# Performance work log

Hardware: AMD Instinct MI355X
Metric: run time of the kernel (lower is better)

Reference implementation:

```python
import jax, jax.numpy as jnp
import numpy as np

ROT = 8
EPS = 1e-5


def _rot_offsets(ks, r):
    # integer-rounded rotated kernel tap offsets, exactly as cal_rot_pad
    c = (ks - 1) / 2
    locx = np.array([[j - c for j in range(ks)] for _ in range(ks)])
    locy = np.array([[i - c for _ in range(ks)] for i in range(ks)])
    loc = np.concatenate((locx.reshape(-1, 1), locy.reshape(-1, 1)), axis=1)  # [ks*ks, (x,y)]
    offs = []
    for i in range(r):
        th = 2.0 * np.pi / r * i
        R = np.array([[np.cos(th), -np.sin(th)], [np.sin(th), np.cos(th)]])
        offs.append(np.around(loc @ R).astype(np.int64))
    m = int(max(int(o.max()) for o in offs))
    return offs, m


def _build_rot_kernel(w, offs, m, r, separate):
    # w: [oc_r, cin, ks, ks]. The torch per-angle pad+cat+1x1conv+crop equals a
    # zero-padded (2m+1)x(2m+1) conv whose kernel scatters w[o,row,col,cin] at
    # (m - y_rot, m - x_rot), accumulating rounding collisions. Non-separate
    # layers cyclically roll the r input-channel blocks by the rotation index.
    oc_r, cin, ks, _ = w.shape
    K = 2 * m + 1
    kers = []
    for i in range(r):
        if separate:
            wi = w
        else:
            wb = w.reshape(oc_r, r, cin // r, ks, ks)
            wi = jnp.roll(wb, i, axis=1).reshape(oc_r, cin, ks, ks)
        wflat = wi.reshape(oc_r, cin, ks * ks)  # row-major tap order matches offs
        l = offs[i]
        ker = jnp.zeros((oc_r, cin, K, K), w.dtype)
        ker = ker.at[:, :, m - l[:, 1], m - l[:, 0]].add(wflat)
        kers.append(ker)
    return jnp.concatenate(kers, axis=0)  # rotation-major out channels, like torch.cat


def _conv(x, w, pad):
    return jax.lax.conv_general_dilated(
        x, w, (1, 1), [(pad, pad), (pad, pad)],
        dimension_numbers=('NCHW', 'OIHW', 'NCHW'))


def _rot_bn(x, gamma, beta, r):
    # training-mode BN applied independently to each rotation chunk, shared params
    B, C, H, W = x.shape
    xs = x.reshape(B, r, C // r, H, W)
    mu = xs.mean(axis=(0, 3, 4), keepdims=True)
    var = xs.var(axis=(0, 3, 4), keepdims=True)
    xn = (xs - mu) * jax.lax.rsqrt(var + EPS)
    xn = xn * gamma[None, None, :, None, None] + beta[None, None, :, None, None]
    return xn.reshape(B, C, H, W)


def _bn(x, gamma, beta):
    mu = x.mean(axis=(0, 2, 3), keepdims=True)
    var = x.var(axis=(0, 2, 3), keepdims=True)
    return (x - mu) * jax.lax.rsqrt(var + EPS) * gamma[None, :, None, None] + beta[None, :, None, None]


def _max_pool(x, k, pad=0):
    return jax.lax.reduce_window(
        x, -jnp.inf, jax.lax.max, (1, 1, k, k), (1, 1, k, k),
        [(0, 0), (0, 0), (pad, pad), (pad, pad)])


def _nms(x, r):
    # note: view is [B, C/r, r, H, W] (rotation-minor), exactly as the torch code
    B, C, H, W = x.shape
    xs = x.reshape(B, C // r, r, H, W)
    y = jnp.max(xs, axis=2, keepdims=True)
    mask = (y != xs).astype(x.dtype)
    return jnp.mean(xs * mask)


def _forward(x, w1, g1, b1, w2, g2, b2, w3, g3, b3,
             w4, g4, b4, w5, g5, b5, w6, g6, b6, w7, b7):
    offs, m = _rot_offsets(3, ROT)  # m == 1 for 3x3
    out = _conv(x, _build_rot_kernel(w1, offs, m, ROT, True), m)
    out = jax.nn.relu(_rot_bn(out, g1, b1, ROT))
    out = _conv(out, _build_rot_kernel(w2, offs, m, ROT, False), m)
    out = jax.nn.relu(_rot_bn(out, g2, b2, ROT))
    out = _max_pool(out, 2)
    out = _conv(out, _build_rot_kernel(w3, offs, m, ROT, False), m)
    out = jax.nn.relu(_rot_bn(out, g3, b3, ROT))
    n = _nms(out, ROT)
    out = jax.nn.relu(_bn(_conv(out, w4, 1), g4, b4))
    out = _max_pool(out, 2)
    out = jax.nn.relu(_bn(_conv(out, w5, 1), g5, b5))
    out = jax.nn.relu(_bn(_conv(out, w6, 1), g6, b6))
    out = _max_pool(out, 2, pad=1)
    out = _conv(out, w7, 2) + b7[None, :, None, None]
    out = _max_pool(out, out.shape[2])  # global max pool
    return out.reshape(out.shape[0], -1), n


def setup_inputs():
    key = jax.random.key(0)
    ks = jax.random.split(key, 24)
    f = jnp.float32
    d = {}
    d['x'] = jax.random.normal(ks[0], (2048, 1, 28, 28), f)
    wshapes = {'w1': (2, 1, 3, 3), 'w2': (2, 16, 3, 3), 'w3': (4, 16, 3, 3),
               'w4': (32, 32, 3, 3), 'w5': (64, 32, 3, 3), 'w6': (64, 64, 3, 3),
               'w7': (10, 64, 4, 4)}
    i = 1
    for name, sh in wshapes.items():
        d[name] = jax.random.normal(ks[i], sh, f) * 0.05
        i += 1
    bnc = {'1': 2, '2': 2, '3': 4, '4': 32, '5': 64, '6': 64}
    for suf, c in bnc.items():
        d['g' + suf] = 1.0 + 0.1 * jax.random.normal(ks[i], (c,), f)
        d['b' + suf] = 0.1 * jax.random.normal(ks[i + 1], (c,), f)
        i += 2
    d['b7'] = 0.1 * jax.random.normal(ks[i], (10,), f)
    return d


def reference(x, w1, w2, w3, w4, w5, w6, w7, g1, b1, g2, b2, g3, b3,
              g4, b4, g5, b5, g6, b6, b7):
    return _forward(x, w1, g1, b1, w2, g2, b2, w3, g3, b3,
                    w4, g4, b4, w5, g5, b5, w6, g6, b6, w7, b7)
```

## Files before the change

kernel.cpp:

```cpp
#include <hip/hip_runtime.h>

static constexpr int NB = 2048;
static constexpr float SENT = -1e30f;

typedef __attribute__((ext_vector_type(8))) short bf16x8;
typedef __attribute__((ext_vector_type(8))) unsigned short u16x8;
typedef __attribute__((ext_vector_type(4))) float f32x4;

#define ST_ADDR(base, ch, kind, copy) ((base) + (((ch)*4 + (copy))*32 + (kind)*8))

static constexpr int DST[8][9] = {
  {8,7,6,5,4,3,2,1,0},
  {5,8,7,2,4,6,1,0,3},
  {2,5,8,1,4,7,0,3,6},
  {1,2,5,0,4,8,3,6,7},
  {0,1,2,3,4,5,6,7,8},
  {3,0,1,6,4,2,7,8,5},
  {6,3,0,7,4,1,8,5,2},
  {7,6,3,8,4,0,5,2,1},
};

__device__ __forceinline__ unsigned short f2bf(float f){
  unsigned int u = __float_as_uint(f);
  u += 0x7fffu + ((u>>16)&1u);
  return (unsigned short)(u>>16);
}

__device__ __forceinline__ float bf2f(unsigned short h){
  return __uint_as_float((unsigned int)h << 16);
}

__device__ __forceinline__ unsigned int cvtpk(float lo, float hi){
  unsigned int r;
  asm("v_cvt_pk_bf16_f32 %0, %1, %2" : "=v"(r) : "v"(lo), "v"(hi));
  return r;
}

__device__ __forceinline__ unsigned int bnpair(unsigned int w, float a0, float b0, float a1, float b1){
  float vlo = __uint_as_float(w << 16);
  float vhi = __uint_as_float(w & 0xFFFF0000u);
  float r0 = fmaxf(vlo*a0 + b0, 0.f);
  float r1 = fmaxf(vhi*a1 + b1, 0.f);
  return cvtpk(r0, r1);
}

__device__ __forceinline__ float st_read(const float* base, int ch, int kind){
  return base[((ch*4+0)*32 + kind*8)] + base[((ch*4+1)*32 + kind*8)]
       + base[((ch*4+2)*32 + kind*8)] + base[((ch*4+3)*32 + kind*8)];
}

__device__ __forceinline__ int border_cell(int t){
  if (t<16) return t;
  if (t<32) return 240 + (t-16);
  if (t<46) return (t-31)*16;
  return (t-45)*16 + 15;
}

__global__ __launch_bounds__(256) void k_pre(const float* __restrict__ x, const float* __restrict__ w1,
                                             const float* __restrict__ w2, const float* __restrict__ w3,
                                             const float* __restrict__ w4,
                                             const float* __restrict__ w5, const float* __restrict__ w6,
                                             const float* __restrict__ w7,
                                             unsigned short* __restrict__ B2,
                                             unsigned short* __restrict__ B3,
                                             unsigned short* __restrict__ wb4,
                                             unsigned short* __restrict__ wb5, unsigned short* __restrict__ wb6,
                                             unsigned short* __restrict__ Bl,
                                             float* __restrict__ st){
  int blk = blockIdx.x;
  if (blk < 283){
    int i = blk*256 + threadIdx.x;
    if (i < 18432){
      int tap = i/2048, rem = i%2048, oc = rem/32, ci = rem%32;
      wb5[i] = f2bf(w5[(oc*32+ci)*9 + tap]);
    } else if (i < 55296){
      int j = i - 18432;
      int tap = j/4096, rem = j%4096, oc = rem/64, ci = rem%64;
      wb6[j] = f2bf(w6[(oc*64+ci)*9 + tap]);
    } else if (i < 64512){
      int j = i - 55296;
      int tap = j/1024, rem = j%1024, oc = rem/32, ci = rem%32;
      wb4[j] = f2bf(w4[(oc*32+ci)*9 + tap]);
    } else if (i < 67072){
      int j = i - 64512;
      int c = j >> 9;
      int rem = j & 511;
      int o = rem >> 5, k = rem & 31;
      int tap = c*2 + (k>>4);
      int ci = k & 15;
      unsigned short v = 0;
      if (tap <= 8){
        int rot = o>>1, u = o&1;
        int bb = ci>>1, ui = ci&1;
        int wc = (((bb - rot) & 7)<<1) | ui;
        int kk = 0;
        #pragma unroll
        for (int q=0;q<9;q++) if (DST[rot][q]==tap) kk=q;
        v = f2bf(w2[(u*16+wc)*9 + kk]);
      }
      B2[j] = v;
    } else if (i < 72192){
      int j = i - 67072;
      int c = j >> 10;
      int rem = j & 1023;
      int o = rem >> 5, k = rem & 31;
      int tap = c*2 + (k>>4);
      int ci = k & 15;
      unsigned short v = 0;
      if (tap <= 8){
        int rot = o>>2, uh = (o>>1)&1, ul = o&1;
        int bb = ci>>1, ui = ci&1;
        int wc = (((bb - rot) & 7)<<1) | ui;
        int kk = 0;
        #pragma unroll
        for (int q=0;q<9;q++) if (DST[rot][q]==tap) kk=q;
        v = f2bf(w3[uh*288 + (ul*16+wc)*9 + kk]);
      }
      B3[j] = v;
    }
    return;
  }
  if (blk < 1307){
    int i = (blk-283)*256 + threadIdx.x;
    int n = i>>10, k = i&1023;
    int pos16 = k>>6, ci = k&63;
    int r = pos16>>2, c = pos16&3;
    unsigned short v = 0;
    if (n < 250){
      int pos = n/10, o = n - 10*(n/10);
      int py = pos/5, px = pos - 5*(pos/5);
      int ky = r - py + 2, kx = c - px + 2;
      if (ky>=0 && ky<4 && kx>=0 && kx<4) v = f2bf(w7[(o*64+ci)*16 + ky*4 + kx]);
    }
    Bl[i] = v;
    return;
  }
  __shared__ float red[4][32];
  float wa[18];
  #pragma unroll
  for (int i=0;i<18;i++) wa[i] = w1[i];
  float s[16], s2[16];
  #pragma unroll
  for (int o=0;o<16;o++){ s[o]=0.f; s2[o]=0.f; }
  for (int idx = (blk-1307)*256 + threadIdx.x; idx < NB*784; idx += 512*256){
    int b = idx/784, pix = idx-b*784;
    int py = pix/28, px = pix-py*28;
    const float* xb = x + (size_t)b*784;
    float tap[9];
    #pragma unroll
    for (int d=0; d<9; d++){
      int dy = d/3-1, dx = d%3-1;
      int yy = py+dy, xx = px+dx;
      tap[d] = (yy>=0 && yy<28 && xx>=0 && xx<28) ? xb[yy*28+xx] : 0.f;
    }
    #pragma unroll
    for (int rot=0; rot<8; rot++){
      #pragma unroll
      for (int u=0; u<2; u++){
        float y = 0.f;
        #pragma unroll
        for (int k=0; k<9; k++) y += wa[u*9+k]*tap[DST[rot][k]];
        int ci = rot*2+u;
        s[ci] += y; s2[ci] += y*y;
      }
    }
  }
  int wid = threadIdx.x>>6;
  #pragma unroll
  for (int o=0;o<16;o++){
    float a = s[o], b2 = s2[o];
    #pragma unroll
    for (int off=32; off; off>>=1){ a += __shfl_down(a,off); b2 += __shfl_down(b2,off); }
    if ((threadIdx.x&63)==0){ red[wid][o] = a; red[wid][16+o] = b2; }
  }
  __syncthreads();
  if (threadIdx.x < 32){
    float v = red[0][threadIdx.x]+red[1][threadIdx.x]+red[2][threadIdx.x]+red[3][threadIdx.x];
    int ch = threadIdx.x & 15, kind = threadIdx.x >> 4;
    atomicAdd(ST_ADDR(st, ch, kind, blk & 3), v);
  }
}

template<int CI>
__global__ __launch_bounds__(64) void k_coef(const float* __restrict__ stin,
                                             const float* __restrict__ g, const float* __restrict__ be,
                                             float invN, int gmask,
                                             float* __restrict__ cf){
  int i = threadIdx.x;
  if (i < CI){
    float mu = st_read(stin, i, 0)*invN;
    float var = st_read(stin, i, 1)*invN - mu*mu;
    float a = g[i & gmask]*rsqrtf(var + 1e-5f);
    cf[i] = a; cf[CI + i] = be[i & gmask] - mu*a;
  }
}

__global__ __launch_bounds__(256, 2) void k_conv2m(const float* __restrict__ x,
                                                   const float* __restrict__ w1,
                                                   const unsigned short* __restrict__ B2,
                                                   const float* __restrict__ stin,
                                                   const float* __restrict__ g1, const float* __restrict__ b1,
                                                   unsigned short* __restrict__ p2b,
                                                   float* __restrict__ stout){
  __shared__ float smemf[8640];
  __shared__ float cab[32];
  __shared__ float red[4][32];
  unsigned short* Ls = (unsigned short*)smemf;
  float* xs = smemf + 7680;
  float* out2 = smemf;
  int t = threadIdx.x;
  int wid = t>>6, lane = t&63;
  int quad = lane>>4, m = lane&15;
  float wa[18];
  #pragma unroll
  for (int i=0;i<18;i++) wa[i] = w1[i];
  if (t < 16){
    const float invN = 1.f/1605632.f;
    float mu = st_read(stin, t, 0)*invN;
    float var = st_read(stin, t, 1)*invN - mu*mu;
    float a = g1[t&1]*rsqrtf(var + 1e-5f);
    cab[t] = a; cab[16+t] = b1[t&1] - mu*a;
  }
  int b = blockIdx.x;
  for (int i=t; i<960; i+=256){
    int r = i>>5, c = i&31;
    int iy = r-1, ix = c-1;
    xs[i] = (iy>=0 && iy<28 && ix>=0 && ix<28) ? x[(size_t)b*784 + iy*28 + ix] : 0.f;
  }
  for (int i=t; i<3840; i+=256) ((unsigned long long*)Ls)[i] = 0ULL;
  __syncthreads();
  for (int i=t; i<784; i+=256){
    int py = i/28, px = i - 28*(i/28);
    float tap[9];
    #pragma unroll
    for (int d=0; d<9; d++) tap[d] = xs[(py + d/3)*32 + px + d%3];
    float y[16];
    #pragma unroll
    for (int rot=0; rot<8; rot++){
      #pragma unroll
      for (int u=0; u<2; u++){
        float acc1 = 0.f;
        #pragma unroll
        for (int k=0; k<9; k++) acc1 += wa[u*9+k]*tap[DST[rot][k]];
        y[rot*2+u] = acc1;
      }
    }
    unsigned long long pk[4];
    #pragma unroll
    for (int q=0; q<4; q++){
      float4 A = *(const float4*)(cab + q*4);
      float4 Bv = *(const float4*)(cab + 16 + q*4);
      float r0 = fmaxf(y[q*4+0]*A.x + Bv.x, 0.f);
      float r1 = fmaxf(y[q*4+1]*A.y + Bv.y, 0.f);
      float r2 = fmaxf(y[q*4+2]*A.z + Bv.z, 0.f);
      float r3 = fmaxf(y[q*4+3]*A.w + Bv.w, 0.f);
      unsigned int lo = cvtpk(r0, r1);
      unsigned int hi = cvtpk(r2, r3);
      pk[q] = (unsigned long long)lo | ((unsigned long long)hi<<32);
    }
    int cell = (py+1)*32 + px + 1;
    unsigned long long* dstp = (unsigned long long*)(Ls + cell*16);
    dstp[0]=pk[0]; dstp[1]=pk[1]; dstp[2]=pk[2]; dstp[3]=pk[3];
  }
  __syncthreads();
  int jb[13];
  #pragma unroll
  for (int j=0;j<13;j++){
    int mt = wid + 4*j;
    int pos = (mt < 49) ? (mt*16 + m) : 0;
    int py = pos/28, px = pos - 28*py;
    jb[j] = (py*32 + px)*16 + (quad&1)*8;
  }
  f32x4 acc[13];
  #pragma unroll
  for (int j=0;j<13;j++) acc[j] = (f32x4){0.f,0.f,0.f,0.f};
  #pragma unroll
  for (int c=0;c<5;c++){
    const int tapA = 2*c, tapB = (2*c+1 < 9) ? 2*c+1 : 8;
    const int offA = ((tapA/3)*32 + tapA%3)*16;
    const int offB = ((tapB/3)*32 + tapB%3)*16;
    int sel = (quad < 2) ? offA : offB;
    bf16x8 Bf = *(const bf16x8*)(B2 + (c*16 + m)*32 + quad*8);
    #pragma unroll
    for (int j=0;j<13;j++){
      int mt = wid + 4*j;
      if (mt >= 49) continue;
      bf16x8 Af = *(const bf16x8*)(Ls + jb[j] + sel);
      acc[j] = __builtin_amdgcn_mfma_f32_16x16x32_bf16(Af, Bf, acc[j], 0, 0, 0);
    }
  }
  __syncthreads();
  float s = 0.f, sq = 0.f;
  #pragma unroll
  for (int j=0;j<13;j++){
    int mt = wid + 4*j;
    if (mt >= 49) continue;
    #pragma unroll
    for (int p=0;p<2;p++){
      int pos0 = mt*16 + quad*4 + p*2;
      float v0 = acc[j][2*p], v1 = acc[j][2*p+1];
      s += v0 + v1; sq += v0*v0 + v1*v1;
      float hm = fmaxf(v0, v1);
      int py = pos0/28, px2 = (pos0 - py*28)>>1;
      out2[(py*14+px2)*17 + m] = hm;
    }
  }
  s += __shfl_down(s,32);  s += __shfl_down(s,16);
  sq += __shfl_down(sq,32); sq += __shfl_down(sq,16);
  if (lane < 16){ red[wid][m] = s; red[wid][16+m] = sq; }
  __syncthreads();
  if (t < 32){
    float v = red[0][t]+red[1][t]+red[2][t]+red[3][t];
    int ch = t & 15, kind = t >> 4;
    atomicAdd(ST_ADDR(stout, ch, kind, b & 3), v);
  }
  unsigned short* pb = p2b + (size_t)b*4096;
  for (int i=t; i<3136; i+=256){
    int cell = i>>4, oc = i&15;
    int yo = cell/14, xo = cell - yo*14;
    float mx = fmaxf(out2[((2*yo)*14+xo)*17 + oc], out2[((2*yo+1)*14+xo)*17 + oc]);
    pb[((yo+1)*16 + xo + 1)*16 + oc] = f2bf(mx);
  }
  for (int i=t; i<960; i+=256){
    int bc = border_cell(i>>4), oc = i&15;
    pb[bc*16 + oc] = f2bf(SENT);
  }
}

__global__ __launch_bounds__(256, 2) void k_conv3w(const unsigned short* __restrict__ p2b,
                                                   const unsigned short* __restrict__ B3,
                                                   const float* __restrict__ stin,
                                                   const float* __restrict__ g2, const float* __restrict__ b2,
                                                   unsigned short* __restrict__ y3b,
                                                   float* __restrict__ stout){
  __shared__ unsigned short act[4][256*24];
  __shared__ float ca[16], cb[16];
  __shared__ float red[4][64];
  int t = threadIdx.x;
  int wid = t>>6, lane = t&63;
  int quad = lane>>4, m = lane&15;
  if (t < 16){
    const float invN = 1.f/1605632.f;
    float mu = st_read(stin, t, 0)*invN;
    float var = st_read(stin, t, 1)*invN - mu*mu;
    float a = g2[t&1]*rsqrtf(var + 1e-5f);
    ca[t] = a; cb[t] = b2[t&1] - mu*a;
  }
  __syncthreads();
  int b = blockIdx.x*4 + wid;
  unsigned short* A = act[wid];
  const unsigned short* sb = p2b + (size_t)b*4096;
  #pragma unroll
  for (int k=0;k<4;k++){
    int cell = lane + 64*k;
    uint4 U0 = *(const uint4*)(sb + cell*16);
    uint4 U1 = *(const uint4*)(sb + cell*16 + 8);
    unsigned int p0 = bnpair(U0.x, ca[0],cb[0], ca[1],cb[1]);
    unsigned int p1 = bnpair(U0.y, ca[2],cb[2], ca[3],cb[3]);
    unsigned int p2 = bnpair(U0.z, ca[4],cb[4], ca[5],cb[5]);
    unsigned int p3 = bnpair(U0.w, ca[6],cb[6], ca[7],cb[7]);
    unsigned int p4 = bnpair(U1.x, ca[8],cb[8], ca[9],cb[9]);
    unsigned int p5 = bnpair(U1.y, ca[10],cb[10], ca[11],cb[11]);
    unsigned int p6 = bnpair(U1.z, ca[12],cb[12], ca[13],cb[13]);
    unsigned int p7 = bnpair(U1.w, ca[14],cb[14], ca[15],cb[15]);
    unsigned long long* q = (unsigned long long*)(A + cell*24);
    q[0] = (unsigned long long)p0 | ((unsigned long long)p1<<32);
    q[1] = (unsigned long long)p2 | ((unsigned long long)p3<<32);
    q[2] = (unsigned long long)p4 | ((unsigned long long)p5<<32);
    q[3] = (unsigned long long)p6 | ((unsigned long long)p7<<32);
  }
  asm volatile("s_waitcnt lgkmcnt(0)" ::: "memory");
  __builtin_amdgcn_sched_barrier(0);
  int jpix[13];
  #pragma unroll
  for (int j=0;j<13;j++){
    int pos = j*16 + m;
    if (pos >= 196) pos = 0;
    int py = pos/14, px = pos - 14*(pos/14);
    jpix[j] = py*16 + px;
  }
  f32x4 acc[13][2];
  #pragma unroll
  for (int j=0;j<13;j++){ acc[j][0] = (f32x4){0,0,0,0}; acc[j][1] = (f32x4){0,0,0,0}; }
  int half = (quad&1)*8;
  #pragma unroll
  for (int c=0;c<5;c++){
    const int tapA = 2*c, tapB = (2*c+1 < 9) ? 2*c+1 : 8;
    const int offA = (tapA/3)*16 + tapA%3;
    const int offB = (tapB/3)*16 + tapB%3;
    int sel = (quad < 2) ? offA : offB;
    bf16x8 Bf0 = *(const bf16x8*)(B3 + (c*32 + m)*32 + quad*8);
    bf16x8 Bf1 = *(const bf16x8*)(B3 + (c*32 + 16 + m)*32 + quad*8);
    #pragma unroll
    for (int j=0;j<13;j++){
      bf16x8 Af = *(const bf16x8*)(A + (jpix[j] + sel)*24 + half);
      acc[j][0] = __builtin_amdgcn_mfma_f32_16x16x32_bf16(Af, Bf0, acc[j][0], 0, 0, 0);
      acc[j][1] = __builtin_amdgcn_mfma_f32_16x16x32_bf16(Af, Bf1, acc[j][1], 0, 0, 0);
    }
  }
  asm volatile("s_waitcnt lgkmcnt(0)" ::: "memory");
  __builtin_amdgcn_sched_barrier(0);
  unsigned short* yb = y3b + (size_t)b*8192;
  float s0=0.f, sq0=0.f, s1=0.f, sq1=0.f;
  #pragma unroll
  for (int j=0;j<13;j++){
    #pragma unroll
    for (int r=0;r<4;r++){
      int pos = j*16 + quad*4 + r;
      if (pos < 196){
        float v0 = acc[j][0][r], v1 = acc[j][1][r];
        int py2 = pos/14, px2 = pos - py2*14;
        int cell = (py2+1)*16 + px2 + 1;
        yb[cell*32 + m]      = f2bf(v0);
        yb[cell*32 + 16 + m] = f2bf(v1);
        s0 += v0; sq0 += v0*v0; s1 += v1; sq1 += v1*v1;
      }
    }
  }
  {
    unsigned short sh = f2bf(SENT);
    unsigned int SP = (unsigned int)sh | ((unsigned int)sh << 16);
    for (int i=lane; i<960; i+=64){
      int bc = border_cell(i>>4);
      int p = i & 15;
      *(unsigned int*)(yb + bc*32 + p*2) = SP;
    }
  }
  s0 += __shfl_down(s0,32); s0 += __shfl_down(s0,16);
  sq0 += __shfl_down(sq0,32); sq0 += __shfl_down(sq0,16);
  s1 += __shfl_down(s1,32); s1 += __shfl_down(s1,16);
  sq1 += __shfl_down(sq1,32); sq1 += __shfl_down(sq1,16);
  if (lane < 16){
    red[wid][m]      = s0;  red[wid][32+m]      = sq0;
    red[wid][16+m]   = s1;  red[wid][32+16+m]   = sq1;
  }
  __syncthreads();
  if (t < 64){
    float v = red[0][t]+red[1][t]+red[2][t]+red[3][t];
    int ch = t & 31, kind = t >> 5;
    atomicAdd(ST_ADDR(stout, ch, kind, blockIdx.x & 3), v);
  }
}

__global__ __launch_bounds__(256, 2) void k_conv4w(const unsigned short* __restrict__ y3b,
                                                   const unsigned short* __restrict__ wb4,
                                                   const float* __restrict__ stin,
                                                   const float* __restrict__ g3, const float* __restrict__ b3,
                                                   float* __restrict__ p4,
                                                   float* __restrict__ stout,
                                                   float* __restrict__ nmsa){
  __shared__ unsigned short act[4][8192];
  __shared__ float ca[32], cb[32];
  __shared__ float red[4][64];
  int t = threadIdx.x;
  int wid = t>>6, lane = t&63;
  int quad = lane>>4, m = lane&15;
  if (t < 32){
    const float invN = 1.f/401408.f;
    float mu = st_read(stin, t, 0)*invN;
    float var = st_read(stin, t, 1)*invN - mu*mu;
    float a = g3[t&3]*rsqrtf(var + 1e-5f);
    ca[t] = a; cb[t] = b3[t&3] - mu*a;
  }
  __syncthreads();
  int b = blockIdx.x*4 + wid;
  unsigned short* A = act[wid];
  const unsigned short* sb = y3b + (size_t)b*8192;
  #pragma unroll
  for (int k=0;k<4;k++){
    int cell = lane + 64*k;
    const uint4* src = (const uint4*)(sb + cell*32);
    int sw = cell & 3;
    unsigned short* dst = A + cell*32;
    #pragma unroll
    for (int c=0;c<4;c++){
      uint4 W = src[c];
      int c0 = c*8;
      unsigned int q0 = bnpair(W.x, ca[c0+0],cb[c0+0], ca[c0+1],cb[c0+1]);
      unsigned int q1 = bnpair(W.y, ca[c0+2],cb[c0+2], ca[c0+3],cb[c0+3]);
      unsigned int q2 = bnpair(W.z, ca[c0+4],cb[c0+4], ca[c0+5],cb[c0+5]);
      unsigned int q3 = bnpair(W.w, ca[c0+6],cb[c0+6], ca[c0+7],cb[c0+7]);
      unsigned long long* q = (unsigned long long*)(dst + ((c ^ sw)<<3));
      q[0] = (unsigned long long)q0 | ((unsigned long long)q1<<32);
      q[1] = (unsigned long long)q2 | ((unsigned long long)q3<<32);
    }
  }
  asm volatile("s_waitcnt lgkmcnt(0)" ::: "memory");
  __builtin_amdgcn_sched_barrier(0);
  float nloc = 0.f;
  for (int i=lane; i<784; i+=64){
    int hw = i>>2, c4 = i&3;
    int cell = (hw/14 + 1)*16 + hw%14 + 1;
    const unsigned int* g32 = (const unsigned int*)(A + cell*32 + ((c4 ^ (cell&3))<<3));
    unsigned int w0 = g32[0], w1 = g32[1], w2 = g32[2], w3 = g32[3];
    float v[8];
    v[0] = __uint_as_float(w0 << 16); v[1] = __uint_as_float(w0 & 0xFFFF0000u);
    v[2] = __uint_as_float(w1 << 16); v[3] = __uint_as_float(w1 & 0xFFFF0000u);
    v[4] = __uint_as_float(w2 << 16); v[5] = __uint_as_float(w2 & 0xFFFF0000u);
    v[6] = __uint_as_float(w3 << 16); v[7] = __uint_as_float(w3 & 0xFFFF0000u);
    float vmax = -1e30f;
    #pragma unroll
    for (int r=0;r<8;r++) vmax = fmaxf(vmax, v[r]);
    #pragma unroll
    for (int r=0;r<8;r++) nloc += (v[r] != vmax) ? v[r] : 0.f;
  }
  #pragma unroll
  for (int off=32; off; off>>=1) nloc += __shfl_down(nloc, off);
  if (lane == 0) atomicAdd(&nmsa[(b & 7)*32], nloc);
  int jc[13], jp[13];
  #pragma unroll
  for (int j=0;j<13;j++){
    int pos = j*16 + m;
    if (pos >= 196) pos = 0;
    int py = pos/14, px = pos - 14*(pos/14);
    jc[j] = py*16 + px;
    jp[j] = px;
  }
  f32x4 acc[13][2];
  #pragma unroll
  for (int j=0;j<13;j++){ acc[j][0] = (f32x4){0,0,0,0}; acc[j][1] = (f32x4){0,0,0,0}; }
  #pragma unroll
  for (int tap=0; tap<9; tap++){
    const int dy = tap/3, dx = tap - 3*(tap/3);
    bf16x8 Bf0 = *(const bf16x8*)(wb4 + (tap*32 + m)*32 + quad*8);
    bf16x8 Bf1 = *(const bf16x8*)(wb4 + (tap*32 + 16 + m)*32 + quad*8);
    #pragma unroll
    for (int j=0;j<13;j++){
      int ci = jc[j] + dy*16 + dx;
      int ph = quad ^ ((jp[j]+dx)&3);
      bf16x8 Af = *(const bf16x8*)(A + ci*32 + ph*8);
      acc[j][0] = __builtin_amdgcn_mfma_f32_16x16x32_bf16(Af, Bf0, acc[j][0], 0, 0, 0);
      acc[j][1] = __builtin_amdgcn_mfma_f32_16x16x32_bf16(Af, Bf1, acc[j][1], 0, 0, 0);
    }
  }
  asm volatile("s_waitcnt lgkmcnt(0)" ::: "memory");
  __builtin_amdgcn_sched_barrier(0);
  float* hp = (float*)A;
  float s0=0.f, sq0=0.f, s1=0.f, sq1=0.f;
  #pragma unroll
  for (int j=0;j<13;j++){
    #pragma unroll
    for (int p=0;p<2;p++){
      int pos0 = j*16 + quad*4 + 2*p;
      if (pos0 + 1 < 196){
        float a0 = acc[j][0][2*p], a1 = acc[j][0][2*p+1];
        float b0 = acc[j][1][2*p], b1 = acc[j][1][2*p+1];
        s0 += a0 + a1; sq0 += a0*a0 + a1*a1;
        s1 += b0 + b1; sq1 += b0*b0 + b1*b1;
        int py0 = pos0/14, pxh = (pos0 - py0*14)>>1;
        hp[(py0*7 + pxh)*33 + m]      = fmaxf(a0, a1);
        hp[(py0*7 + pxh)*33 + 16 + m] = fmaxf(b0, b1);
      }
    }
  }
  s0 += __shfl_down(s0,32); s0 += __shfl_down(s0,16);
  sq0 += __shfl_down(sq0,32); sq0 += __shfl_down(sq0,16);
  s1 += __shfl_down(s1,32); s1 += __shfl_down(s1,16);
  sq1 += __shfl_down(sq1,32); sq1 += __shfl_down(sq1,16);
  if (lane < 16){
    red[wid][m]      = s0;  red[wid][32+m]      = sq0;
    red[wid][16+m]   = s1;  red[wid][32+16+m]   = sq1;
  }
  asm volatile("s_waitcnt lgkmcnt(0)" ::: "memory");
  __builtin_amdgcn_sched_barrier(0);
  for (int i=lane; i<1568; i+=64){
    int cell = i>>5, oc = i&31;
    int yo = cell/7, xo = cell - yo*7;
    float mx = fmaxf(hp[((2*yo)*7 + xo)*33 + oc], hp[((2*yo+1)*7 + xo)*33 + oc]);
    p4[((size_t)b*49 + cell)*32 + oc] = mx;
  }
  __syncthreads();
  if (t < 64){
    float v = red[0][t]+red[1][t]+red[2][t]+red[3][t];
    int ch = t & 31, kind = t >> 5;
    atomicAdd(ST_ADDR(stout, ch, kind, blockIdx.x & 3), v);
  }
}

template<int CI>
__global__ __launch_bounds__(256, 2) void k_conv56m(const float* __restrict__ src,
                                                    const unsigned short* __restrict__ wb,
                                                    const float* __restrict__ stin,
                                                    const float* __restrict__ g, const float* __restrict__ be,
                                                    float invN,
                                                    float* __restrict__ dst,
                                                    float* __restrict__ stout){
  constexpr int CIP = CI + 8;
  constexpr int KC = CI/32;
  __shared__ unsigned short lin[4][81*CIP];
  __shared__ float red[4][256];
  __shared__ float ca[CI], cb[CI];
  int wid = threadIdx.x>>6, lane = threadIdx.x&63;
  int quad = lane>>4, m = lane&15;
  unsigned short* L = lin[wid];
  if (threadIdx.x < CI){
    int i = threadIdx.x;
    float mu = st_read(stin, i, 0)*invN;
    float var = st_read(stin, i, 1)*invN - mu*mu;
    float a = g[i]*rsqrtf(var + 1e-5f);
    ca[i] = a; cb[i] = be[i] - mu*a;
  }
  for (int i = lane; i < 81*CIP/4; i += 64) ((unsigned long long*)L)[i] = 0ULL;
  __syncthreads();
  int b = blockIdx.x*4 + wid;
  const float* sb = src + (size_t)b*49*CI;
  for (int i = lane; i < 49*CI/4; i += 64){
    int pos = i/(CI/4), cig = i - pos*(CI/4);
    float4 v = *(const float4*)(sb + pos*CI + cig*4);
    float r0 = fmaxf(v.x*ca[cig*4]  +cb[cig*4],   0.f);
    float r1 = fmaxf(v.y*ca[cig*4+1]+cb[cig*4+1], 0.f);
    float r2 = fmaxf(v.z*ca[cig*4+2]+cb[cig*4+2], 0.f);
    float r3 = fmaxf(v.w*ca[cig*4+3]+cb[cig*4+3], 0.f);
    int pos9 = (pos/7 + 1)*9 + pos%7 + 1;
    unsigned int lo = cvtpk(r0, r1);
    unsigned int hi = cvtpk(r2, r3);
    *(unsigned long long*)(L + pos9*CIP + cig*4) =
        (unsigned long long)lo | ((unsigned long long)hi<<32);
  }
  __syncthreads();
  int py[4], px[4];
  #pragma unroll
  for (int mt=0; mt<4; mt++){
    int pos = mt*16 + m;
    if (pos < 49){ py[mt] = pos/7; px[mt] = pos%7; }
    else { py[mt] = 0; px[mt] = 0; }
  }
  f32x4 acc[4][4];
  #pragma unroll
  for (int nt=0; nt<4; nt++)
    #pragma unroll
    for (int mt=0; mt<4; mt++) acc[nt][mt] = (f32x4){0.f,0.f,0.f,0.f};

  for (int tap=0; tap<9; tap++){
    int dy = tap/3, dx = tap - dy*3;
    int o9[4];
    #pragma unroll
    for (int mt=0; mt<4; mt++) o9[mt] = ((py[mt]+dy)*9 + px[mt]+dx)*CIP;
    #pragma unroll
    for (int kc=0; kc<KC; kc++){
      int ko = kc*32 + quad*8;
      bf16x8 Bf[4], Af[4];
      #pragma unroll
      for (int nt=0; nt<4; nt++)
        Bf[nt] = *(const bf16x8*)(wb + (tap*64 + nt*16 + m)*CI + ko);
      #pragma unroll
      for (int mt=0; mt<4; mt++)
        Af[mt] = *(const bf16x8*)(L + o9[mt] + ko);
      #pragma unroll
      for (int nt=0; nt<4; nt++)
        #pragma unroll
        for (int mt=0; mt<4; mt++)
          acc[nt][mt] = __builtin_amdgcn_mfma_f32_16x16x32_bf16(Af[mt], Bf[nt], acc[nt][mt], 0, 0, 0);
    }
  }
  float* db = dst + (size_t)b*49*64;
  float snt[4], sqnt[4];
  #pragma unroll
  for (int nt=0; nt<4; nt++){
    float s = 0.f, sq = 0.f;
    #pragma unroll
    for (int mt=0; mt<4; mt++){
      #pragma unroll
      for (int r=0; r<4; r++){
        int pos = mt*16 + quad*4 + r;
        if (pos < 49){
          float v = acc[nt][mt][r];
          db[pos*64 + nt*16 + m] = v;
          s += v; sq += v*v;
        }
      }
    }
    s += __shfl_down(s, 32);  s += __shfl_down(s, 16);
    sq += __shfl_down(sq, 32); sq += __shfl_down(sq, 16);
    snt[nt] = s; sqnt[nt] = sq;
  }
  if (lane < 16){
    #pragma unroll
    for (int nt=0; nt<4; nt++){
      red[wid][nt*16 + lane] = snt[nt];
      red[wid][128 + nt*16 + lane] = sqnt[nt];
    }
  }
  __syncthreads();
  if (threadIdx.x < 128){
    int c = threadIdx.x & 63;
    int off = (threadIdx.x < 64) ? threadIdx.x : (128 + c);
    float v = red[0][off]+red[1][off]+red[2][off]+red[3][off];
    int kind = (threadIdx.x < 64) ? 0 : 1;
    atomicAdd(ST_ADDR(stout, c, kind, blockIdx.x & 3), v);
  }
}

__global__ __launch_bounds__(256) void k_pool6(const float* __restrict__ y,
                                               const float* __restrict__ cf,
                                               unsigned short* __restrict__ p6b){
  int idx = blockIdx.x*256 + threadIdx.x;
  int oc = idx & 63; int t2 = idx >> 6;
  int xo = t2 & 3;  int yo = (t2>>2) & 3;  int b = t2 >> 4;
  float a = cf[oc];
  float bo = cf[64 + oc];
  const float* src = y + (size_t)b*3136;
  float mx = -1e30f;
  #pragma unroll
  for (int dy=0;dy<2;dy++){
    int iy = yo*2 - 1 + dy;
    if (iy < 0 || iy >= 7) continue;
    #pragma unroll
    for (int dx=0;dx<2;dx++){
      int ix = xo*2 - 1 + dx;
      if (ix < 0 || ix >= 7) continue;
      mx = fmaxf(mx, src[(iy*7+ix)*64 + oc]*a + bo);
    }
  }
  p6b[(size_t)b*1024 + (yo*4 + xo)*64 + oc] = f2bf(fmaxf(mx, 0.f));
}

__global__ __launch_bounds__(256) void k_gemm7(const unsigned short* __restrict__ A,
                                               const unsigned short* __restrict__ Bl,
                                               float* __restrict__ part){
  __shared__ float Lw[4][16*65];
  int wid = threadIdx.x>>6, lane = threadIdx.x&63;
  int quad = lane>>4, m = lane&15;
  int blkm = blockIdx.x >> 2, blkn = blockIdx.x & 3;
  int rowb = blkm*64 + wid*16 + m;
  const unsigned short* Arow = A + (size_t)rowb*1024;
  f32x4 acc[4];
  #pragma unroll
  for (int nt=0; nt<4; nt++) acc[nt] = (f32x4){0.f,0.f,0.f,0.f};
  for (int kc=0; kc<32; kc++){
    bf16x8 Af = *(const bf16x8*)(Arow + kc*32 + quad*8);
    #pragma unroll
    for (int nt=0; nt<4; nt++){
      bf16x8 Bf = *(const bf16x8*)(Bl + (size_t)(blkn*64 + nt*16 + m)*1024 + kc*32 + quad*8);
      acc[nt] = __builtin_amdgcn_mfma_f32_16x16x32_bf16(Af, Bf, acc[nt], 0, 0, 0);
    }
  }
  float* Lp = &Lw[wid][0];
  #pragma unroll
  for (int nt=0; nt<4; nt++)
    #pragma unroll
    for (int r=0; r<4; r++)
      Lp[(quad*4+r)*65 + nt*16 + m] = acc[nt][r];
  __syncthreads();
  for (int i=lane; i<160; i+=64){
    int br = i/10, o = i - 10*(i/10);
    int c0 = ((o - blkn*64) % 10 + 10) % 10;
    float mx = -1e30f;
    for (int c=c0; c<64; c+=10){
      if (blkn*64 + c < 250) mx = fmaxf(mx, Lp[br*65 + c]);
    }
    part[((size_t)(blkm*64 + wid*16 + br)*4 + blkn)*10 + o] = mx;
  }
}

__global__ __launch_bounds__(256) void k_logits(const float* __restrict__ part,
                                                const float* __restrict__ bias,
                                                const float* __restrict__ nmsa,
                                                float* __restrict__ out){
  int idx = blockIdx.x*256 + threadIdx.x;
  int b = idx/10, o = idx - 10*(idx/10);
  const float* p = part + (size_t)b*40 + o;
  float mx = fmaxf(fmaxf(p[0], p[10]), fmaxf(p[20], p[30]));
  out[idx] = mx + bias[o];
  if (blockIdx.x == 0 && threadIdx.x == 0){
    float nm = 0.f;
    #pragma unroll
    for (int cp=0; cp<8; cp++) nm += nmsa[cp*32];
    out[20480] = nm * (1.f/12845056.f);
  }
}

extern "C" void kernel_launch(void* const* d_in, const int* in_sizes, int n_in,
                              void* d_out, int out_size, void* d_ws, size_t ws_size,
                              hipStream_t stream){
  const float* x  = (const float*)d_in[0];
  const float* w1 = (const float*)d_in[1];
  const float* w2 = (const float*)d_in[2];
  const float* w3 = (const float*)d_in[3];
  const float* w4 = (const float*)d_in[4];
  const float* w5 = (const float*)d_in[5];
  const float* w6 = (const float*)d_in[6];
  const float* w7 = (const float*)d_in[7];
  const float* g1 = (const float*)d_in[8];
  const float* b1 = (const float*)d_in[9];
  const float* g2 = (const float*)d_in[10];
  const float* b2 = (const float*)d_in[11];
  const float* g3 = (const float*)d_in[12];
  const float* b3 = (const float*)d_in[13];
  const float* g4 = (const float*)d_in[14];
  const float* b4 = (const float*)d_in[15];
  const float* g5 = (const float*)d_in[16];
  const float* b5 = (const float*)d_in[17];
  const float* g6 = (const float*)d_in[18];
  const float* b6 = (const float*)d_in[19];
  const float* b7 = (const float*)d_in[20];
  float* out = (float*)d_out;
  float* W = (float*)d_ws;

  unsigned short* p2b = (unsigned short*)(W + 15728640);
  unsigned short* y3b = (unsigned short*)(W + 24117248);
  float* p4   = W + 0;
  float* st   = W + 3211264;
  float* nmsa = st + 6*8192;
  float* cf6  = nmsa + 256;
  float* y5   = W + 3407872;
  float* y6   = W + 10223616;
  unsigned short* p6b = (unsigned short*)(W + 16646144);
  unsigned short* wb5 = (unsigned short*)(W + 40894464);
  unsigned short* wb6 = (unsigned short*)(W + 40912896);
  unsigned short* wb4 = (unsigned short*)(W + 40931328);
  unsigned short* Bl = (unsigned short*)(W + 40951808);
  float* part = W + 41082880;
  unsigned short* B2 = (unsigned short*)(W + 41164800);
  unsigned short* B3 = (unsigned short*)(W + 41166080);

  hipMemsetAsync(st, 0, 49536*sizeof(float), stream);

  k_pre<<<1819,256,0,stream>>>(x, w1, w2, w3, w4, w5, w6, w7,
                               B2, B3, wb4, wb5, wb6, Bl, st + 0*8192);

  k_conv2m<<<2048,256,0,stream>>>(x, w1, B2, st + 0*8192, g1, b1, p2b, st + 1*8192);

  k_conv3w<<<512,256,0,stream>>>(p2b, B3, st + 1*8192, g2, b2, y3b, st + 2*8192);

  k_conv4w<<<512,256,0,stream>>>(y3b, wb4, st + 2*8192, g3, b3, p4, st + 3*8192, nmsa);

  k_conv56m<32><<<512,256,0,stream>>>(p4, wb5, st + 3*8192, g4, b4, 1.f/401408.f, y5, st + 4*8192);

  k_conv56m<64><<<512,256,0,stream>>>(y5, wb6, st + 4*8192, g5, b5, 1.f/100352.f, y6, st + 5*8192);

  k_coef<64><<<1,64,0,stream>>>(st + 5*8192, g6, b6, 1.f/100352.f, 63, cf6);

  k_pool6<<<8192,256,0,stream>>>(y6, cf6, p6b);

  k_gemm7<<<128,256,0,stream>>>(p6b, Bl, part);
  k_logits<<<80,256,0,stream>>>(part, b7, nmsa, out);
}
```

Baseline: 263.5 us.

## Split conv2 into per-wave row bands to drop block-wide barriers

```diff
diff --git a/kernel.cpp b/kernel.cpp
--- a/kernel.cpp
+++ b/kernel.cpp
@@ -195,19 +195,17 @@
   }
 }
 
-__global__ __launch_bounds__(256, 2) void k_conv2m(const float* __restrict__ x,
+__global__ __launch_bounds__(256, 2) void k_conv2w(const float* __restrict__ x,
                                                    const float* __restrict__ w1,
                                                    const unsigned short* __restrict__ B2,
                                                    const float* __restrict__ stin,
                                                    const float* __restrict__ g1, const float* __restrict__ b1,
                                                    unsigned short* __restrict__ p2b,
                                                    float* __restrict__ stout){
-  __shared__ float smemf[8640];
+  __shared__ unsigned short act[4][7680];
+  __shared__ float xsw[4][384];
   __shared__ float cab[32];
   __shared__ float red[4][32];
-  unsigned short* Ls = (unsigned short*)smemf;
-  float* xs = smemf + 7680;
-  float* out2 = smemf;
   int t = threadIdx.x;
   int wid = t>>6, lane = t&63;
   int quad = lane>>4, m = lane&15;
@@ -221,89 +219,113 @@
     float a = g1[t&1]*rsqrtf(var + 1e-5f);
     cab[t] = a; cab[16+t] = b1[t&1] - mu*a;
   }
+  __syncthreads();
   int b = blockIdx.x;
-  for (int i=t; i<960; i+=256){
-    int r = i>>5, c = i&31;
-    int iy = r-1, ix = c-1;
+  int r0 = 8*wid;
+  int nrows = (wid<3) ? 8 : 4;
+  unsigned short* A = act[wid];
+  float* xs = xsw[wid];
+  for (int i=lane; i<(nrows+4)*32; i+=64){
+    int lr = i>>5, c = i&31;
+    int iy = r0-2+lr, ix = c-1;
     xs[i] = (iy>=0 && iy<28 && ix>=0 && ix<28) ? x[(size_t)b*784 + iy*28 + ix] : 0.f;
   }
-  for (int i=t; i<3840; i+=256) ((unsigned long long*)Ls)[i] = 0ULL;
-  __syncthreads();
-  for (int i=t; i<784; i+=256){
-    int py = i/28, px = i - 28*(i/28);
-    float tap[9];
-    #pragma unroll
-    for (int d=0; d<9; d++) tap[d] = xs[(py + d/3)*32 + px + d%3];
-    float y[16];
-    #pragma unroll
-    for (int rot=0; rot<8; rot++){
+  asm volatile("s_waitcnt lgkmcnt(0)" ::: "memory");
+  __builtin_amdgcn_sched_barrier(0);
+  for (int i=lane; i<(nrows+2)*2; i+=64){
+    int lr = i>>1, scol = (i&1) ? 29 : 0;
+    unsigned long long* q = (unsigned long long*)(A + (lr*32 + scol)*24);
+    q[0]=0; q[1]=0; q[2]=0; q[3]=0;
+  }
+  for (int i=lane; i<(nrows+2)*28; i+=64){
+    int lr = i/28, px = i - 28*lr;
+    int py = r0-1+lr;
+    unsigned long long pk[4] = {0ULL,0ULL,0ULL,0ULL};
+    if (py >= 0 && py < 28){
+      float tap[9];
       #pragma unroll
-      for (int u=0; u<2; u++){
-        float acc1 = 0.f;
+      for (int d=0; d<9; d++) tap[d] = xs[(lr + d/3)*32 + px + d%3];
+      float y[16];
+      #pragma unroll
+      for (int rot=0; rot<8; rot++){
         #pragma unroll
-        for (int k=0; k<9; k++) acc1 += wa[u*9+k]*tap[DST[rot][k]];
-        y[rot*2+u] = acc1;
+        for (int u=0; u<2; u++){
+          float acc1 = 0.f;
+          #pragma unroll
+          for (int k=0; k<9; k++) acc1 += wa[u*9+k]*tap[DST[rot][k]];
+          y[rot*2+u] = acc1;
+        }
       }
-    }
-    unsigned long long pk[4];
-    #pragma unroll
-    for (int q=0; q<4; q++){
-      float4 A = *(const float4*)(cab + q*4);
-      float4 Bv = *(const float4*)(cab + 16 + q*4);
-      float r0 = fmaxf(y[q*4+0]*A.x + Bv.x, 0.f);
-      float r1 = fmaxf(y[q*4+1]*A.y + Bv.y, 0.f);
-      float r2 = fmaxf(y[q*4+2]*A.z + Bv.z, 0.f);
-      float r3 = fmaxf(y[q*4+3]*A.w + Bv.w, 0.f);
-      unsigned int lo = cvtpk(r0, r1);
-      unsigned int hi = cvtpk(r2, r3);
-      pk[q] = (unsigned long long)lo | ((unsigned long long)hi<<32);
-    }
-    int cell = (py+1)*32 + px + 1;
-    unsigned long long* dstp = (unsigned long long*)(Ls + cell*16);
-    dstp[0]=pk[0]; dstp[1]=pk[1]; dstp[2]=pk[2]; dstp[3]=pk[3];
-  }
-  __syncthreads();
-  int jb[13];
-  #pragma unroll
-  for (int j=0;j<13;j++){
-    int mt = wid + 4*j;
-    int pos = (mt < 49) ? (mt*16 + m) : 0;
-    int py = pos/28, px = pos - 28*py;
-    jb[j] = (py*32 + px)*16 + (quad&1)*8;
-  }
-  f32x4 acc[13];
-  #pragma unroll
-  for (int j=0;j<13;j++) acc[j] = (f32x4){0.f,0.f,0.f,0.f};
+      #pragma unroll
+      for (int q=0; q<4; q++){
+        float4 Aa = *(const float4*)(cab + q*4);
+        float4 Bv = *(const float4*)(cab + 16 + q*4);
+        float r0f = fmaxf(y[q*4+0]*Aa.x + Bv.x, 0.f);
+        float r1f = fmaxf(y[q*4+1]*Aa.y + Bv.y, 0.f);
+        float r2f = fmaxf(y[q*4+2]*Aa.z + Bv.z, 0.f);
+        float r3f = fmaxf(y[q*4+3]*Aa.w + Bv.w, 0.f);
+        unsigned int lo = cvtpk(r0f, r1f);
+        unsigned int hi = cvtpk(r2f, r3f);
+        pk[q] = (unsigned long long)lo | ((unsigned long long)hi<<32);
+      }
+    }
+    unsigned long long* q = (unsigned long long*)(A + (lr*32 + px + 1)*24);
+    q[0]=pk[0]; q[1]=pk[1]; q[2]=pk[2]; q[3]=pk[3];
+  }
+  asm volatile("s_waitcnt lgkmcnt(0)" ::: "memory");
+  __builtin_amdgcn_sched_barrier(0);
+  int njt = (wid<3) ? 14 : 7;
+  int jb[14];
+  #pragma unroll
+  for (int j=0;j<14;j++){
+    int posl = j*16 + m;
+    if (posl >= nrows*28) posl = 0;
+    int py = posl/28, px = posl - 28*py;
+    jb[j] = (py*32 + px)*24 + (quad&1)*8;
+  }
+  f32x4 acc[14];
+  #pragma unroll
+  for (int j=0;j<14;j++) acc[j] = (f32x4){0.f,0.f,0.f,0.f};
   #pragma unroll
   for (int c=0;c<5;c++){
     const int tapA = 2*c, tapB = (2*c+1 < 9) ? 2*c+1 : 8;
-    const int offA = ((tapA/3)*32 + tapA%3)*16;
-    const int offB = ((tapB/3)*32 + tapB%3)*16;
+    const int offA = ((tapA/3)*32 + tapA%3)*24;
+    const int offB = ((tapB/3)*32 + tapB%3)*24;
     int sel = (quad < 2) ? offA : offB;
     bf16x8 Bf = *(const bf16x8*)(B2 + (c*16 + m)*32 + quad*8);
     #pragma unroll
-    for (int j=0;j<13;j++){
-      int mt = wid + 4*j;
-      if (mt >= 49) continue;
-      bf16x8 Af = *(const bf16x8*)(Ls + jb[j] + sel);
+    for (int j=0;j<14;j++){
+      if (j >= njt) continue;
+      bf16x8 Af = *(const bf16x8*)(A + jb[j] + sel);
       acc[j] = __builtin_amdgcn_mfma_f32_16x16x32_bf16(Af, Bf, acc[j], 0, 0, 0);
     }
   }
-  __syncthreads();
+  asm volatile("s_waitcnt lgkmcnt(0)" ::: "memory");
+  __builtin_amdgcn_sched_barrier(0);
+  float* hp = (float*)A;
   float s = 0.f, sq = 0.f;
   #pragma unroll
-  for (int j=0;j<13;j++){
-    int mt = wid + 4*j;
-    if (mt >= 49) continue;
+  for (int j=0;j<14;j++){
+    if (j >= njt) continue;
     #pragma unroll
     for (int p=0;p<2;p++){
-      int pos0 = mt*16 + quad*4 + p*2;
+      int posl = j*16 + quad*4 + 2*p;
       float v0 = acc[j][2*p], v1 = acc[j][2*p+1];
       s += v0 + v1; sq += v0*v0 + v1*v1;
       float hm = fmaxf(v0, v1);
-      int py = pos0/28, px2 = (pos0 - py*28)>>1;
-      out2[(py*14+px2)*17 + m] = hm;
-    }
+      int py = posl/28, px2 = (posl - py*28)>>1;
+      hp[(py*14 + px2)*17 + m] = hm;
+    }
+  }
+  asm volatile("s_waitcnt lgkmcnt(0)" ::: "memory");
+  __builtin_amdgcn_sched_barrier(0);
+  unsigned short* pb = p2b + (size_t)b*4096;
+  for (int i=lane; i<(nrows>>1)*14*16; i+=64){
+    int cell = i>>4, oc = i&15;
+    int yol = cell/14, xo = cell - yol*14;
+    float mx = fmaxf(hp[((2*yol)*14+xo)*17 + oc], hp[((2*yol+1)*14+xo)*17 + oc]);
+    int yo = (r0>>1) + yol;
+    pb[((yo+1)*16 + xo + 1)*16 + oc] = f2bf(mx);
   }
   s += __shfl_down(s,32);  s += __shfl_down(s,16);
   sq += __shfl_down(sq,32); sq += __shfl_down(sq,16);
@@ -313,13 +335,6 @@
     float v = red[0][t]+red[1][t]+red[2][t]+red[3][t];
     int ch = t & 15, kind = t >> 4;
     atomicAdd(ST_ADDR(stout, ch, kind, b & 3), v);
-  }
-  unsigned short* pb = p2b + (size_t)b*4096;
-  for (int i=t; i<3136; i+=256){
-    int cell = i>>4, oc = i&15;
-    int yo = cell/14, xo = cell - yo*14;
-    float mx = fmaxf(out2[((2*yo)*14+xo)*17 + oc], out2[((2*yo+1)*14+xo)*17 + oc]);
-    pb[((yo+1)*16 + xo + 1)*16 + oc] = f2bf(mx);
   }
   for (int i=t; i<960; i+=256){
     int bc = border_cell(i>>4), oc = i&15;
@@ -819,7 +834,7 @@
   k_pre<<<1819,256,0,stream>>>(x, w1, w2, w3, w4, w5, w6, w7,
                                B2, B3, wb4, wb5, wb6, Bl, st + 0*8192);
 
-  k_conv2m<<<2048,256,0,stream>>>(x, w1, B2, st + 0*8192, g1, b1, p2b, st + 1*8192);
+  k_conv2w<<<2048,256,0,stream>>>(x, w1, B2, st + 0*8192, g1, b1, p2b, st + 1*8192);
 
   k_conv3w<<<512,256,0,stream>>>(p2b, B3, st + 1*8192, g2, b2, y3b, st + 2*8192);
 
```

Result: slower. 284.2 us (+7.9%).
